# Kernel optimization log

Measured on AMD Instinct MI355X. Metric: run time of the kernel, lower is better.

Reference implementation:

```python
import jax, jax.numpy as jnp
import numpy as np

IN_CH = 64
NODE = 48
K_NEIGS = 10
KERNEL = 5
STRIDE = 2
BN_EPS = 1e-5


def _local_kernel(size, k, s):
    idx = np.arange(size * size).reshape(size, size)
    win = np.lib.stride_tricks.sliding_window_view(idx, (k, k))[::s, ::s]
    patches = win.reshape(-1, k * k)  # [n_edges, k*k] pixel indices
    n_edges = patches.shape[0]
    H = np.zeros((size * size, n_edges), dtype=np.float32)
    H[patches.reshape(-1), np.repeat(np.arange(n_edges), k * k)] = 1.0
    return jnp.asarray(H)


def _pairwise_distance(x):
    # (B,N,C) -> (B,N,N) squared euclidean
    xsq = jnp.sum(x * x, axis=-1, keepdims=True)
    return xsq - 2.0 * jnp.einsum('bnc,bmc->bnm', x, x) + jnp.swapaxes(xsq, 1, 2)


def _batched_knn(x, k):
    d = _pairwise_distance(x)
    avg = d.mean(-1, keepdims=True)
    neg_vals, inds = jax.lax.top_k(-d, k + 1)  # smallest k+1, sorted ascending
    return -neg_vals, inds, d, avg


def _incidence(inds, N):
    # weights_function(prob=False) == ones; scatter ones then transpose
    B, _, K = inds.shape
    b = jnp.arange(B)[:, None, None]
    p = jnp.arange(N)[None, :, None]
    M = jnp.zeros((B, N, N), dtype=jnp.float32).at[b, p, inds].set(1.0)
    return jnp.swapaxes(M, 1, 2)


def _generate_G(H):
    # G = diag(DV^-0.5) @ H @ I @ diag(DE^-1) @ H^T @ diag(DV^-0.5)
    DV = H.sum(axis=2)  # (B,N)
    DE = H.sum(axis=1)  # (B,E)
    dv2 = DV ** -0.5
    Hs = H * (1.0 / DE)[:, None, :]
    M = jnp.einsum('bne,bme->bnm', Hs, H)
    return dv2[:, :, None] * M * dv2[:, None, :]


def _build_G(x, local_H):
    B, N, C = x.shape
    _, topk_inds, _, _ = _batched_knn(x, K_NEIGS)
    H1 = _incidence(topk_inds, N)
    Dv = H1.sum(axis=2, keepdims=True)  # alpha = 1.0
    max_k = int(jnp.max(Dv))  # data-dependent width (eager, matches torch)
    _, ti2, _, _ = _batched_knn(x, max_k - 1)  # (B,N,max_k)
    tk = jnp.arange(max_k)[None, None, :]
    rng = jnp.broadcast_to(jnp.arange(N)[None, :, None], (B, N, max_k))
    new_inds = jnp.where(tk >= Dv, rng, ti2)
    new_H = _incidence(new_inds, N)
    loc = jnp.broadcast_to(local_H[None], (B,) + local_H.shape)
    return _generate_G(jnp.concatenate([new_H, loc], axis=2))


def _hgnn(x, G, W, b, gamma, beta):
    h = jnp.einsum('bnc,oc->bno', x, W) + b  # Linear
    h = jnp.einsum('bnm,bmc->bnc', G, h)
    mean = h.mean(axis=(0, 1))  # BatchNorm1d over (B,N) per channel
    var = h.var(axis=(0, 1))
    h = gamma * (h - mean) / jnp.sqrt(var + BN_EPS) + beta
    return jax.nn.relu(h) + x


def setup_inputs() -> dict:
    key = jax.random.key(0)
    k1, k2, k3 = jax.random.split(key, 3)
    B, N, C = 4, NODE * NODE, IN_CH
    x = jax.random.normal(k1, (B, N, C), dtype=jnp.float32)
    W = jax.random.normal(k2, (C, C), dtype=jnp.float32) / np.sqrt(C)
    b = jax.random.normal(k3, (C,), dtype=jnp.float32) * 0.01
    gamma = jnp.ones((C,), dtype=jnp.float32)
    beta = jnp.zeros((C,), dtype=jnp.float32)
    return {"x": x, "W": W, "b": b, "gamma": gamma, "beta": beta}


def reference(x, W, b, gamma, beta):
    local_H = _local_kernel(NODE, KERNEL, STRIDE)
    G = _build_G(x, local_H)  # graph construction is no_grad in torch
    return _hgnn(x, G, W, b, gamma, beta)
```

## Files before the change

kernel.cpp:

```cpp
#include <hip/hip_runtime.h>


#define HB    4
#define HN    2304
#define HC    64
#define HK    11
#define HL    48
#define HW    22
#define HE2   484
#define HE    (HN + HE2)
#define HRPB  4
#define NSLOT 36
#define NPAIRS (HB * HK * HN)

__global__ void hg14_sentinel(float* out, int n) {
    int i = blockIdx.x * 256 + threadIdx.x;
    if (i < n) out[i] = 12345.0f;
}

__global__ void hg14_init(int* Dv, int* indeg, float* bnsum, float* bnss) {
    int i = blockIdx.x * 256 + threadIdx.x;
    if (i < HB * HN) { Dv[i] = 0; indeg[i] = 0; }
    if (i < HC) { bnsum[i] = 0.f; bnss[i] = 0.f; }
}

__global__ __launch_bounds__(64) void hg14_linear(const float* x, const float* W,
                                                  const float* bias, float* h1,
                                                  float* xsq, float* xT) {
    int row = blockIdx.x;
    int t = threadIdx.x;
    __shared__ float xr[HC];
    float v = x[row * HC + t];
    xr[t] = v;
    __syncthreads();
    float sq = v * v;
    #pragma unroll
    for (int o = 32; o > 0; o >>= 1) sq += __shfl_xor(sq, o);
    if (t == 0) xsq[row] = sq;
    int b = row / HN, n = row % HN;
    xT[(b * HC + t) * HN + n] = v;
    float acc = bias[t];
    #pragma unroll 8
    for (int c = 0; c < HC; c++) acc += xr[c] * W[t * HC + c];
    h1[row * HC + t] = acc;
}

__device__ __forceinline__ unsigned hg14_wave_min_u32(unsigned v) {
    #pragma unroll
    for (int o = 32; o > 0; o >>= 1) {
        unsigned ov = __shfl_xor(v, o);
        v = ov < v ? ov : v;
    }
    return v;
}

#define HG14_INS4(q0, q1, q2, q3, x)                                     \
    {                                                                    \
        unsigned long long x_ = (x), n_;                                 \
        n_ = q0 < x_ ? q0 : x_; x_ = q0 < x_ ? x_ : q0; q0 = n_;         \
        n_ = q1 < x_ ? q1 : x_; x_ = q1 < x_ ? x_ : q1; q1 = n_;         \
        n_ = q2 < x_ ? q2 : x_; x_ = q2 < x_ ? x_ : q2; q2 = n_;         \
        if (x_ < q3) q3 = x_;                                            \
    }

#define HG14_CE(u, v)                                                    \
    { unsigned long long t_ = u < v ? u : v; v = u < v ? v : u; u = t_; }

#define HG14_BUILD()                                                               \
    {                                                                              \
        unsigned long long a0 = CINF, a1 = CINF, a2 = CINF, a3 = CINF;             \
        unsigned long long b0 = CINF, b1 = CINF, b2 = CINF, b3 = CINF;             \
        _Pragma("unroll")                                                          \
        for (int s = 0; s < NSLOT / 2; s++) {                                      \
            unsigned long long pa = ((unsigned long long)key[s] << 12) |           \
                                    (unsigned)((s << 6) | lane);                   \
            unsigned long long pb = ((unsigned long long)key[s + 18] << 12) |      \
                                    (unsigned)(((s + 18) << 6) | lane);            \
            HG14_INS4(a0, a1, a2, a3, pa);                                         \
            HG14_INS4(b0, b1, b2, b3, pb);                                         \
        }                                                                          \
        c0 = a0 < b3 ? a0 : b3; c1 = a1 < b2 ? a1 : b2;                            \
        c2 = a2 < b1 ? a2 : b1; c3 = a3 < b0 ? a3 : b0;                            \
        HG14_CE(c0, c2); HG14_CE(c1, c3); HG14_CE(c0, c1); HG14_CE(c2, c3);        \
    }

#define HG14_EXTRACT(kk, EMIT)                                                     \
    {                                                                              \
        for (int j = 0; j < (kk); j++) {                                           \
            unsigned hk = (unsigned)(c0 >> 12);                                    \
            unsigned mk = hg14_wave_min_u32(hk);                                   \
            unsigned long long bal = __ballot(hk == mk);                           \
            bool iswin;                                                            \
            if (__popcll(bal) == 1) {                                              \
                iswin = (hk == mk);                                                \
            } else {                                                               \
                unsigned mc = (hk == mk) ? (unsigned)(c0 & 0xFFFu) : 0xFFFFFFFFu;  \
                unsigned mm = hg14_wave_min_u32(mc);                               \
                iswin = (mc == mm);                                                \
            }                                                                      \
            if (iswin) {                                                           \
                int bi = (int)(c0 & 0xFFFu);                                       \
                EMIT;                                                              \
                unsigned long long popped = c0;                                    \
                c0 = c1; c1 = c2; c2 = c3; c3 = CINF;                              \
                if (c0 == CINF) {                                                  \
                    _Pragma("unroll")                                              \
                    for (int s = 0; s < NSLOT; s++) {                              \
                        unsigned long long pk =                                    \
                            ((unsigned long long)key[s] << 12) |                   \
                            (unsigned)((s << 6) | lane);                           \
                        if (pk > popped) HG14_INS4(c0, c1, c2, c3, pk);            \
                    }                                                              \
                }                                                                  \
            }                                                                      \
        }                                                                          \
    }

__device__ __forceinline__ void hg14_kth(const unsigned (&key)[NSLOT], int kk,
                                         unsigned& T, int& cntLess, int& take) {
    unsigned andv = 0xFFFFFFFFu, orv = 0u;
    #pragma unroll
    for (int s = 0; s < NSLOT; s++) { andv &= key[s]; orv |= key[s]; }
    #pragma unroll
    for (int o = 32; o > 0; o >>= 1) {
        andv &= (unsigned)__shfl_xor((int)andv, o);
        orv  |= (unsigned)__shfl_xor((int)orv, o);
    }
    unsigned diff = andv ^ orv;
    if (diff == 0u) { T = andv; cntLess = 0; take = kk; return; }
    int tstart = 31 - __builtin_clz(diff);
    unsigned lowmask = (tstart == 31) ? 0xFFFFFFFFu : ((1u << (tstart + 1)) - 1u);
    unsigned pref = andv & ~lowmask;
    int r = kk;
    for (int t = tstart; t >= 0; t--) {
        unsigned pt = pref >> t;
        int c = 0;
        #pragma unroll
        for (int s = 0; s < NSLOT; s++) c += ((key[s] >> t) == pt) ? 1 : 0;
        #pragma unroll
        for (int o = 32; o > 0; o >>= 1) c += __shfl_xor(c, o);
        if (r > c) { r -= c; pref |= (1u << t); }
    }
    T = pref; cntLess = kk - r; take = r;
}

__device__ __forceinline__ void hg14_scan64(int v, int lane, int& excl, int& total) {
    int inc = v;
    #pragma unroll
    for (int o = 1; o < 64; o <<= 1) {
        int u = __shfl_up(inc, o);
        if (lane >= o) inc += u;
    }
    excl = inc - v;
    total = __shfl(inc, 63);
}

__global__ __launch_bounds__(256) void hg14_knn_count(const float* xT, const float* xsq,
                                                      int* Dv, unsigned int* kcache,
                                                      int storekeys) {
    __shared__ float d[HRPB][HN];
    __shared__ __align__(16) float xrt[HC][HRPB];
    const int t = threadIdx.x;
    const int b = blockIdx.x / (HN / HRPB);
    const int n0 = (blockIdx.x % (HN / HRPB)) * HRPB;
    const int r = t >> 6;
    const int lane = t & 63;
    xrt[lane][r] = xT[(b * HC + lane) * HN + n0 + r];
    __syncthreads();
    float xs[HRPB];
    #pragma unroll
    for (int q = 0; q < HRPB; q++) xs[q] = xsq[b * HN + n0 + q];

    #pragma unroll
    for (int i = 0; i < 4; i++) {
        const int m = 512 * i + 2 * t;
        float2 d0 = {0.f, 0.f}, d1 = {0.f, 0.f}, d2 = {0.f, 0.f}, d3 = {0.f, 0.f};
        #pragma unroll 8
        for (int c = 0; c < HC; c++) {
            float4 xq = *reinterpret_cast<const float4*>(&xrt[c][0]);
            float2 xv = *reinterpret_cast<const float2*>(&xT[(b * HC + c) * HN + m]);
            d0.x += xq.x * xv.x; d0.y += xq.x * xv.y;
            d1.x += xq.y * xv.x; d1.y += xq.y * xv.y;
            d2.x += xq.z * xv.x; d2.y += xq.z * xv.y;
            d3.x += xq.w * xv.x; d3.y += xq.w * xv.y;
        }
        float s0 = xsq[b * HN + m], s1 = xsq[b * HN + m + 1];
        *reinterpret_cast<float2*>(&d[0][m]) =
            make_float2(xs[0] + s0 - 2.f * d0.x, xs[0] + s1 - 2.f * d0.y);
        *reinterpret_cast<float2*>(&d[1][m]) =
            make_float2(xs[1] + s0 - 2.f * d1.x, xs[1] + s1 - 2.f * d1.y);
        *reinterpret_cast<float2*>(&d[2][m]) =
            make_float2(xs[2] + s0 - 2.f * d2.x, xs[2] + s1 - 2.f * d2.y);
        *reinterpret_cast<float2*>(&d[3][m]) =
            make_float2(xs[3] + s0 - 2.f * d3.x, xs[3] + s1 - 2.f * d3.y);
    }
    {
        const int m = 2048 + t;
        float d0 = 0.f, d1 = 0.f, d2 = 0.f, d3 = 0.f;
        #pragma unroll 8
        for (int c = 0; c < HC; c++) {
            float4 xq = *reinterpret_cast<const float4*>(&xrt[c][0]);
            float xv = xT[(b * HC + c) * HN + m];
            d0 += xq.x * xv; d1 += xq.y * xv; d2 += xq.z * xv; d3 += xq.w * xv;
        }
        float sm = xsq[b * HN + m];
        d[0][m] = xs[0] + sm - 2.f * d0;
        d[1][m] = xs[1] + sm - 2.f * d1;
        d[2][m] = xs[2] + sm - 2.f * d2;
        d[3][m] = xs[3] + sm - 2.f * d3;
    }
    __syncthreads();

    const int p = n0 + r;
    const unsigned long long CINF = ~0ull;
    unsigned int key[NSLOT];
    unsigned long long c0, c1, c2, c3;
    const int rowbase = (b * HN + p) * NSLOT;
    #pragma unroll
    for (int s = 0; s < NSLOT; s++) {
        float f = d[r][(s << 6) | lane];
        unsigned int ub = __float_as_uint(f);
        unsigned int k = ub ^ (((unsigned int)(((int)ub) >> 31)) | 0x80000000u);
        key[s] = k;
        if (storekeys) kcache[(rowbase + s) * 64 + lane] = k;
    }
    HG14_BUILD();
    HG14_EXTRACT(HK, atomicAdd(&Dv[b * HN + bi], 1));
}

__global__ __launch_bounds__(256) void hg14_scan(const int* Dv, int* offs) {
    __shared__ int part[256];
    int t = threadIdx.x;
    int base = t * 36;
    int s = 0;
    for (int i = 0; i < 36; i++) s += max(Dv[base + i], 1);
    part[t] = s;
    __syncthreads();
    if (t == 0) { int acc = 0; for (int i = 0; i < 256; i++) { int v = part[i]; part[i] = acc; acc += v; } }
    __syncthreads();
    int acc = part[t];
    for (int i = 0; i < 36; i++) { offs[base + i] = acc; acc += max(Dv[base + i], 1); }
}

__device__ __forceinline__ void hg14_select_emit(const unsigned (&key)[NSLOT],
                                                 int b, int p, int lane, int kk, int base,
                                                 int* indeg, unsigned int* pairs) {
    unsigned T; int cntLess, take;
    hg14_kth(key, kk, T, cntLess, take);
    int cl = 0;
    #pragma unroll
    for (int s = 0; s < NSLOT; s++) cl += (key[s] < T) ? 1 : 0;
    int off, tot;
    hg14_scan64(cl, lane, off, tot);
    int w = 0;
    #pragma unroll
    for (int s = 0; s < NSLOT; s++) {
        if (key[s] < T) {
            int m = (s << 6) | lane;
            atomicAdd(&indeg[b * HN + m], 1);
            pairs[base + off + w] =
                ((unsigned)b << 24) | ((unsigned)p << 12) | (unsigned)m;
            w++;
        }
    }
    int lastm = -1;
    for (int t2 = 0; t2 < take; t2++) {
        int mc = 0x7FFFFFFF;
        #pragma unroll
        for (int s = 0; s < NSLOT; s++) {
            int m = (s << 6) | lane;
            if (key[s] == T && m > lastm && m < mc) mc = m;
        }
        int mmin = mc;
        #pragma unroll
        for (int o = 32; o > 0; o >>= 1) {
            int ov = __shfl_xor(mmin, o);
            mmin = ov < mmin ? ov : mmin;
        }
        if (mc == mmin) {
            atomicAdd(&indeg[b * HN + mmin], 1);
            pairs[base + cntLess + t2] =
                ((unsigned)b << 24) | ((unsigned)p << 12) | (unsigned)mmin;
        }
        lastm = mmin;
    }
}

__global__ __launch_bounds__(256) void hg14_knn_sel_cached(const unsigned int* kcache,
                                                           const int* Dv, const int* offs,
                                                           int* indeg, unsigned int* pairs) {
    const int t = threadIdx.x;
    const int lane = t & 63;
    const int gw = blockIdx.x * HRPB + (t >> 6);
    const int b = gw / HN, p = gw % HN;
    unsigned int key[NSLOT];
    const int rowbase = gw * NSLOT;
    #pragma unroll
    for (int s = 0; s < NSLOT; s++) key[s] = kcache[(rowbase + s) * 64 + lane];
    hg14_select_emit(key, b, p, lane, max(Dv[gw], 1), offs[gw], indeg, pairs);
}

__global__ __launch_bounds__(256) void hg14_knn_sel_full(const float* xT, const float* xsq,
                                                         const int* Dv, const int* offs,
                                                         int* indeg, unsigned int* pairs) {
    __shared__ float d[HRPB][HN];
    __shared__ float xr[HRPB][HC];
    const int t = threadIdx.x;
    const int b = blockIdx.x / (HN / HRPB);
    const int n0 = (blockIdx.x % (HN / HRPB)) * HRPB;
    const int r = t >> 6;
    const int lane = t & 63;
    xr[r][lane] = xT[(b * HC + lane) * HN + n0 + r];
    __syncthreads();
    float xs[HRPB];
    #pragma unroll
    for (int q = 0; q < HRPB; q++) xs[q] = xsq[b * HN + n0 + q];
    for (int m = t; m < HN; m += 256) {
        float dot0 = 0.f, dot1 = 0.f, dot2 = 0.f, dot3 = 0.f;
        #pragma unroll 8
        for (int c = 0; c < HC; c++) {
            float xv = xT[(b * HC + c) * HN + m];
            dot0 += xr[0][c] * xv;
            dot1 += xr[1][c] * xv;
            dot2 += xr[2][c] * xv;
            dot3 += xr[3][c] * xv;
        }
        float xsm = xsq[b * HN + m];
        d[0][m] = xs[0] + xsm - 2.f * dot0;
        d[1][m] = xs[1] + xsm - 2.f * dot1;
        d[2][m] = xs[2] + xsm - 2.f * dot2;
        d[3][m] = xs[3] + xsm - 2.f * dot3;
    }
    __syncthreads();
    const int p = n0 + r;
    unsigned int key[NSLOT];
    #pragma unroll
    for (int s = 0; s < NSLOT; s++) {
        float f = d[r][(s << 6) | lane];
        unsigned int ub = __float_as_uint(f);
        key[s] = ub ^ (((unsigned int)(((int)ub) >> 31)) | 0x80000000u);
    }
    const int gw = b * HN + p;
    hg14_select_emit(key, b, p, lane, max(Dv[gw], 1), offs[gw], indeg, pairs);
}

__device__ __forceinline__ int hg14_lo(int rc) { return max(0, (rc - 3) / 2); }
__device__ __forceinline__ int hg14_hi(int rc) { return min(HW - 1, rc / 2); }

__global__ __launch_bounds__(256) void hg14_scale(float* h1, const int* indeg) {
    int i = blockIdx.x * 256 + threadIdx.x;
    int node = i >> 6;
    int n = node % HN;
    int r = n / HL, c = n % HL;
    int cover = max(0, hg14_hi(r) - hg14_lo(r) + 1) * max(0, hg14_hi(c) - hg14_lo(c) + 1);
    int dvn = max(indeg[node] + cover, 1);
    h1[i] *= rsqrtf((float)dvn);
}

__global__ void hg14_zero(float* z, float* h2) {
    int i = blockIdx.x * 256 + threadIdx.x;
    int b = i / (HN * HC), rem = i % (HN * HC);
    z[b * HE * HC + rem] = 0.f;
    h2[i] = 0.f;
}

__global__ __launch_bounds__(256) void hg14_edge(const unsigned int* pairs, const int* Dv,
                                                 const float* y, float* z) {
    int wv = (blockIdx.x * 256 + threadIdx.x) >> 6;
    int lane = threadIdx.x & 63;
    if (wv < NPAIRS) {
        unsigned int pk = pairs[wv];
        int b = pk >> 24;
        if (b >= HB) return;
        int p = (pk >> 12) & 0xFFF, m = pk & 0xFFF;
        float invde = 1.f / (float)max(Dv[b * HN + p], 1);
        atomicAdd(&z[(b * HE + p) * HC + lane], y[(b * HN + m) * HC + lane] * invde);
    } else {
        int w2 = wv - NPAIRS;
        if (w2 >= HB * HE2) return;
        int b = w2 / HE2, w = w2 % HE2;
        int wr = w / HW, wc = w % HW;
        float acc = 0.f;
        #pragma unroll
        for (int i = 0; i < 5; i++)
            #pragma unroll
            for (int j = 0; j < 5; j++)
                acc += y[(b * HN + (wr * 2 + i) * HL + wc * 2 + j) * HC + lane];
        z[(b * HE + HN + w) * HC + lane] = acc * (1.f / 25.f);
    }
}

__global__ __launch_bounds__(256) void hg14_gscatter(const unsigned int* pairs,
                                                     const float* z, float* h2) {
    int idx = (blockIdx.x * 256 + threadIdx.x) >> 6;
    int lane = threadIdx.x & 63;
    if (idx >= NPAIRS) return;
    unsigned int pk = pairs[idx];
    int b = pk >> 24;
    if (b >= HB) return;
    int p = (pk >> 12) & 0xFFF, m = pk & 0xFFF;
    atomicAdd(&h2[(b * HN + m) * HC + lane], z[(b * HE + p) * HC + lane]);
}

__global__ __launch_bounds__(256) void hg14_gfinish(const float* z, const int* indeg, float* h2) {
    int wave = (blockIdx.x * 256 + threadIdx.x) >> 6;
    int lane = threadIdx.x & 63;
    int b = wave / HN, n = wave % HN;
    int g = b * HN + n;
    float acc = h2[g * HC + lane];
    int r = n / HL, c = n % HL;
    int rlo = hg14_lo(r), rhi = hg14_hi(r), clo = hg14_lo(c), chi = hg14_hi(c);
    for (int wr = rlo; wr <= rhi; wr++)
        for (int wc = clo; wc <= chi; wc++)
            acc += z[(b * HE + HN + wr * HW + wc) * HC + lane];
    int dvn = max(indeg[g] + max(0, rhi - rlo + 1) * max(0, chi - clo + 1), 1);
    h2[g * HC + lane] = acc * rsqrtf((float)dvn);
}

__global__ __launch_bounds__(256) void hg14_bnstats(const float* h2, float* bnsum, float* bnss) {
    int t = threadIdx.x;
    int c = t & 63, rg = t >> 6;
    int row0 = blockIdx.x * 36;
    float s = 0.f, ss = 0.f;
    for (int r = rg; r < 36; r += 4) {
        float v = h2[(row0 + r) * HC + c];
        s += v; ss += v * v;
    }
    __shared__ float ls[256], lss[256];
    ls[t] = s; lss[t] = ss;
    __syncthreads();
    if (t < 64) {
        s  = ls[t]  + ls[t + 64]  + ls[t + 128]  + ls[t + 192];
        ss = lss[t] + lss[t + 64] + lss[t + 128] + lss[t + 192];
        atomicAdd(&bnsum[t], s);
        atomicAdd(&bnss[t], ss);
    }
}

__global__ __launch_bounds__(256) void hg14_final(const float* h2, const float* x,
                                                  const float* gamma, const float* beta,
                                                  const float* bnsum, const float* bnss,
                                                  float* out) {
    int i = blockIdx.x * 256 + threadIdx.x;
    int c = i & 63;
    const float M = (float)(HB * HN);
    float mean = bnsum[c] / M;
    float var  = bnss[c] / M - mean * mean;
    float inv  = rsqrtf(var + 1e-5f);
    float h = gamma[c] * (h2[i] - mean) * inv + beta[c];
    out[i] = fmaxf(h, 0.f) + x[i];
}

extern "C" void kernel_launch(void* const* d_in, const int* in_sizes, int n_in,
                              void* d_out, int out_size, void* d_ws, size_t ws_size,
                              hipStream_t stream) {
    const float* x     = (const float*)d_in[0];
    const float* W     = (const float*)d_in[1];
    const float* bias  = (const float*)d_in[2];
    const float* gamma = (const float*)d_in[3];
    const float* beta  = (const float*)d_in[4];
    float* out = (float*)d_out;
    (void)in_sizes; (void)n_in;

    char* ws = (char*)d_ws;
    size_t off = 0;
    float*        xsq     = (float*)(ws + off);        off += (size_t)HB * HN * 4;
    float*        h1      = (float*)(ws + off);        off += (size_t)HB * HN * HC * 4;
    float*        h2      = (float*)(ws + off);        off += (size_t)HB * HN * HC * 4;
    int*          Dv      = (int*)(ws + off);          off += (size_t)HB * HN * 4;
    int*          indeg   = (int*)(ws + off);          off += (size_t)HB * HN * 4;
    int*          offs    = (int*)(ws + off);          off += (size_t)HB * HN * 4;
    unsigned int* pairs   = (unsigned int*)(ws + off); off += (size_t)NPAIRS * 4;
    float*        bnsum   = (float*)(ws + off);        off += 256;
    float*        bnss    = (float*)(ws + off);        off += 256;
    float*        xT      = (float*)(ws + off);
    float*        z       = (float*)(ws + off);
    off += (size_t)HB * HE * HC * 4;
    size_t base_need = off;
    unsigned int* kcache  = (unsigned int*)(ws + off);
    size_t cache_need = off + (size_t)HB * HN * NSLOT * 64 * 4;

    if (ws_size < base_need) {
        hg14_sentinel<<<(out_size + 255) / 256, 256, 0, stream>>>(out, out_size);
        return;
    }
    const int use_cache = (ws_size >= cache_need) ? 1 : 0;

    const int EDGE_WAVES = NPAIRS + HB * HE2;

    hg14_init<<<(HB * HN + 255) / 256, 256, 0, stream>>>(Dv, indeg, bnsum, bnss);
    hg14_linear<<<HB * HN, 64, 0, stream>>>(x, W, bias, h1, xsq, xT);
    hg14_knn_count<<<HB * (HN / HRPB), 256, 0, stream>>>(xT, xsq, Dv, kcache, use_cache);
    hg14_scan<<<1, 256, 0, stream>>>(Dv, offs);
    if (use_cache)
        hg14_knn_sel_cached<<<HB * (HN / HRPB), 256, 0, stream>>>(kcache, Dv, offs, indeg, pairs);
    else
        hg14_knn_sel_full<<<HB * (HN / HRPB), 256, 0, stream>>>(xT, xsq, Dv, offs, indeg, pairs);
    hg14_scale<<<(HB * HN * HC) / 256, 256, 0, stream>>>(h1, indeg);
    hg14_zero<<<(HB * HN * HC) / 256, 256, 0, stream>>>(z, h2);
    hg14_edge<<<EDGE_WAVES / 4, 256, 0, stream>>>(pairs, Dv, h1, z);
    hg14_gscatter<<<(NPAIRS * 64) / 256, 256, 0, stream>>>(pairs, z, h2);
    hg14_gfinish<<<(HB * HN) / 4, 256, 0, stream>>>(z, indeg, h2);
    hg14_bnstats<<<256, 256, 0, stream>>>(h2, bnsum, bnss);
    hg14_final<<<(HB * HN * HC) / 256, 256, 0, stream>>>(h2, x, gamma, beta, bnsum, bnss, out);
}
```

Before: 375.2 us.

## Cache per-row top-192 candidates instead of full distance keys for KNN selection

Instead of writing all 2304 sort keys per row to a global cache and rereading them in the selection pass, the count kernel now picks the 192 smallest keys per row and stores them packed with their column indices. The selection kernel reads only those 192 candidates. Rows whose degree exceeds the cap fall back to a kernel that recomputes the distances. The scale and zero kernels are also merged into one prep kernel. This cuts global traffic in the select pass, at the cost of extra kth-selection work in the count kernel and an extra, mostly idle, fallback launch.

```diff
diff --git a/kernel.cpp b/kernel.cpp
--- a/kernel.cpp
+++ b/kernel.cpp
@@ -11,20 +11,21 @@
 #define HE    (HN + HE2)
 #define HRPB  4
 #define NSLOT 36
+#define HCAP  192
 #define NPAIRS (HB * HK * HN)
 
-__global__ void hg14_sentinel(float* out, int n) {
+__global__ void hg16_sentinel(float* out, int n) {
     int i = blockIdx.x * 256 + threadIdx.x;
     if (i < n) out[i] = 12345.0f;
 }
 
-__global__ void hg14_init(int* Dv, int* indeg, float* bnsum, float* bnss) {
+__global__ void hg16_init(int* Dv, int* indeg, float* bnsum, float* bnss) {
     int i = blockIdx.x * 256 + threadIdx.x;
     if (i < HB * HN) { Dv[i] = 0; indeg[i] = 0; }
     if (i < HC) { bnsum[i] = 0.f; bnss[i] = 0.f; }
 }
 
-__global__ __launch_bounds__(64) void hg14_linear(const float* x, const float* W,
+__global__ __launch_bounds__(64) void hg16_linear(const float* x, const float* W,
                                                   const float* bias, float* h1,
                                                   float* xsq, float* xT) {
     int row = blockIdx.x;
@@ -45,7 +46,7 @@
     h1[row * HC + t] = acc;
 }
 
-__device__ __forceinline__ unsigned hg14_wave_min_u32(unsigned v) {
+__device__ __forceinline__ unsigned hg16_wave_min_u32(unsigned v) {
     #pragma unroll
     for (int o = 32; o > 0; o >>= 1) {
         unsigned ov = __shfl_xor(v, o);
@@ -54,7 +55,7 @@
     return v;
 }
 
-#define HG14_INS4(q0, q1, q2, q3, x)                                     \
+#define HG16_INS4(q0, q1, q2, q3, x)                                     \
     {                                                                    \
         unsigned long long x_ = (x), n_;                                 \
         n_ = q0 < x_ ? q0 : x_; x_ = q0 < x_ ? x_ : q0; q0 = n_;         \
@@ -63,10 +64,10 @@
         if (x_ < q3) q3 = x_;                                            \
     }
 
-#define HG14_CE(u, v)                                                    \
+#define HG16_CE(u, v)                                                    \
     { unsigned long long t_ = u < v ? u : v; v = u < v ? v : u; u = t_; }
 
-#define HG14_BUILD()                                                               \
+#define HG16_BUILD()                                                               \
     {                                                                              \
         unsigned long long a0 = CINF, a1 = CINF, a2 = CINF, a3 = CINF;             \
         unsigned long long b0 = CINF, b1 = CINF, b2 = CINF, b3 = CINF;             \
@@ -76,26 +77,26 @@
                                     (unsigned)((s << 6) | lane);                   \
             unsigned long long pb = ((unsigned long long)key[s + 18] << 12) |      \
                                     (unsigned)(((s + 18) << 6) | lane);            \
-            HG14_INS4(a0, a1, a2, a3, pa);                                         \
-            HG14_INS4(b0, b1, b2, b3, pb);                                         \
+            HG16_INS4(a0, a1, a2, a3, pa);                                         \
+            HG16_INS4(b0, b1, b2, b3, pb);                                         \
         }                                                                          \
         c0 = a0 < b3 ? a0 : b3; c1 = a1 < b2 ? a1 : b2;                            \
         c2 = a2 < b1 ? a2 : b1; c3 = a3 < b0 ? a3 : b0;                            \
-        HG14_CE(c0, c2); HG14_CE(c1, c3); HG14_CE(c0, c1); HG14_CE(c2, c3);        \
-    }
-
-#define HG14_EXTRACT(kk, EMIT)                                                     \
+        HG16_CE(c0, c2); HG16_CE(c1, c3); HG16_CE(c0, c1); HG16_CE(c2, c3);        \
+    }
+
+#define HG16_EXTRACT(kk, EMIT)                                                     \
     {                                                                              \
         for (int j = 0; j < (kk); j++) {                                           \
             unsigned hk = (unsigned)(c0 >> 12);                                    \
-            unsigned mk = hg14_wave_min_u32(hk);                                   \
+            unsigned mk = hg16_wave_min_u32(hk);                                   \
             unsigned long long bal = __ballot(hk == mk);                           \
             bool iswin;                                                            \
             if (__popcll(bal) == 1) {                                              \
                 iswin = (hk == mk);                                                \
             } else {                                                               \
                 unsigned mc = (hk == mk) ? (unsigned)(c0 & 0xFFFu) : 0xFFFFFFFFu;  \
-                unsigned mm = hg14_wave_min_u32(mc);                               \
+                unsigned mm = hg16_wave_min_u32(mc);                               \
                 iswin = (mc == mm);                                                \
             }                                                                      \
             if (iswin) {                                                           \
@@ -109,18 +110,19 @@
                         unsigned long long pk =                                    \
                             ((unsigned long long)key[s] << 12) |                   \
                             (unsigned)((s << 6) | lane);                           \
-                        if (pk > popped) HG14_INS4(c0, c1, c2, c3, pk);            \
+                        if (pk > popped) HG16_INS4(c0, c1, c2, c3, pk);            \
                     }                                                              \
                 }                                                                  \
             }                                                                      \
         }                                                                          \
     }
 
-__device__ __forceinline__ void hg14_kth(const unsigned (&key)[NSLOT], int kk,
+template <int NS>
+__device__ __forceinline__ void hg16_kth(const unsigned (&key)[NS], int kk,
                                          unsigned& T, int& cntLess, int& take) {
     unsigned andv = 0xFFFFFFFFu, orv = 0u;
     #pragma unroll
-    for (int s = 0; s < NSLOT; s++) { andv &= key[s]; orv |= key[s]; }
+    for (int s = 0; s < NS; s++) { andv &= key[s]; orv |= key[s]; }
     #pragma unroll
     for (int o = 32; o > 0; o >>= 1) {
         andv &= (unsigned)__shfl_xor((int)andv, o);
@@ -136,7 +138,7 @@
         unsigned pt = pref >> t;
         int c = 0;
         #pragma unroll
-        for (int s = 0; s < NSLOT; s++) c += ((key[s] >> t) == pt) ? 1 : 0;
+        for (int s = 0; s < NS; s++) c += ((key[s] >> t) == pt) ? 1 : 0;
         #pragma unroll
         for (int o = 32; o > 0; o >>= 1) c += __shfl_xor(c, o);
         if (r > c) { r -= c; pref |= (1u << t); }
@@ -144,7 +146,7 @@
     T = pref; cntLess = kk - r; take = r;
 }
 
-__device__ __forceinline__ void hg14_scan64(int v, int lane, int& excl, int& total) {
+__device__ __forceinline__ void hg16_scan64(int v, int lane, int& excl, int& total) {
     int inc = v;
     #pragma unroll
     for (int o = 1; o < 64; o <<= 1) {
@@ -155,9 +157,8 @@
     total = __shfl(inc, 63);
 }
 
-__global__ __launch_bounds__(256) void hg14_knn_count(const float* xT, const float* xsq,
-                                                      int* Dv, unsigned int* kcache,
-                                                      int storekeys) {
+__global__ __launch_bounds__(256) void hg16_knn_count(const float* xT, const float* xsq,
+                                                      int* Dv, unsigned long long* topc) {
     __shared__ float d[HRPB][HN];
     __shared__ __align__(16) float xrt[HC][HRPB];
     const int t = threadIdx.x;
@@ -212,23 +213,56 @@
     __syncthreads();
 
     const int p = n0 + r;
+    const int gw = b * HN + p;
     const unsigned long long CINF = ~0ull;
     unsigned int key[NSLOT];
     unsigned long long c0, c1, c2, c3;
-    const int rowbase = (b * HN + p) * NSLOT;
     #pragma unroll
     for (int s = 0; s < NSLOT; s++) {
         float f = d[r][(s << 6) | lane];
         unsigned int ub = __float_as_uint(f);
-        unsigned int k = ub ^ (((unsigned int)(((int)ub) >> 31)) | 0x80000000u);
-        key[s] = k;
-        if (storekeys) kcache[(rowbase + s) * 64 + lane] = k;
-    }
-    HG14_BUILD();
-    HG14_EXTRACT(HK, atomicAdd(&Dv[b * HN + bi], 1));
-}
-
-__global__ __launch_bounds__(256) void hg14_scan(const int* Dv, int* offs) {
+        key[s] = ub ^ (((unsigned int)(((int)ub) >> 31)) | 0x80000000u);
+    }
+    HG16_BUILD();
+    HG16_EXTRACT(HK, atomicAdd(&Dv[b * HN + bi], 1));
+    unsigned T; int cntLess, take;
+    hg16_kth<NSLOT>(key, HCAP, T, cntLess, take);
+    int cl = 0;
+    #pragma unroll
+    for (int s = 0; s < NSLOT; s++) cl += (key[s] < T) ? 1 : 0;
+    int off, tot;
+    hg16_scan64(cl, lane, off, tot);
+    unsigned long long* tb = topc + (size_t)gw * HCAP;
+    int w = 0;
+    #pragma unroll
+    for (int s = 0; s < NSLOT; s++) {
+        if (key[s] < T) {
+            tb[off + w] = ((unsigned long long)key[s] << 12)
+                        | (unsigned)((s << 6) | lane);
+            w++;
+        }
+    }
+    int lastm = -1;
+    for (int t2 = 0; t2 < take; t2++) {
+        int mc = 0x7FFFFFFF;
+        #pragma unroll
+        for (int s = 0; s < NSLOT; s++) {
+            int m = (s << 6) | lane;
+            if (key[s] == T && m > lastm && m < mc) mc = m;
+        }
+        int mmin = mc;
+        #pragma unroll
+        for (int o = 32; o > 0; o >>= 1) {
+            int ov = __shfl_xor(mmin, o);
+            mmin = ov < mmin ? ov : mmin;
+        }
+        if (mc == mmin)
+            tb[cntLess + t2] = ((unsigned long long)T << 12) | (unsigned)mmin;
+        lastm = mmin;
+    }
+}
+
+__global__ __launch_bounds__(256) void hg16_scan(const int* Dv, int* offs) {
     __shared__ int part[256];
     int t = threadIdx.x;
     int base = t * 36;
@@ -242,21 +276,35 @@
     for (int i = 0; i < 36; i++) { offs[base + i] = acc; acc += max(Dv[base + i], 1); }
 }
 
-__device__ __forceinline__ void hg14_select_emit(const unsigned (&key)[NSLOT],
-                                                 int b, int p, int lane, int kk, int base,
-                                                 int* indeg, unsigned int* pairs) {
+__global__ __launch_bounds__(256) void hg16_sel_top(const unsigned long long* topc,
+                                                    const int* Dv, const int* offs,
+                                                    int* indeg, unsigned int* pairs) {
+    const int t = threadIdx.x;
+    const int lane = t & 63;
+    const int gw = blockIdx.x * HRPB + (t >> 6);
+    const int b = gw / HN, p = gw % HN;
+    const int kk = max(Dv[gw], 1);
+    if (kk > HCAP) return;
+    unsigned long long pk[3];
+    unsigned key[3];
+    #pragma unroll
+    for (int s = 0; s < 3; s++) {
+        pk[s] = topc[(size_t)gw * HCAP + (s << 6) + lane];
+        key[s] = (unsigned)(pk[s] >> 12);
+    }
     unsigned T; int cntLess, take;
-    hg14_kth(key, kk, T, cntLess, take);
+    hg16_kth<3>(key, kk, T, cntLess, take);
+    const int base = offs[gw];
     int cl = 0;
     #pragma unroll
-    for (int s = 0; s < NSLOT; s++) cl += (key[s] < T) ? 1 : 0;
+    for (int s = 0; s < 3; s++) cl += (key[s] < T) ? 1 : 0;
     int off, tot;
-    hg14_scan64(cl, lane, off, tot);
+    hg16_scan64(cl, lane, off, tot);
     int w = 0;
     #pragma unroll
-    for (int s = 0; s < NSLOT; s++) {
+    for (int s = 0; s < 3; s++) {
         if (key[s] < T) {
-            int m = (s << 6) | lane;
+            int m = (int)(pk[s] & 0xFFFu);
             atomicAdd(&indeg[b * HN + m], 1);
             pairs[base + off + w] =
                 ((unsigned)b << 24) | ((unsigned)p << 12) | (unsigned)m;
@@ -267,8 +315,8 @@
     for (int t2 = 0; t2 < take; t2++) {
         int mc = 0x7FFFFFFF;
         #pragma unroll
-        for (int s = 0; s < NSLOT; s++) {
-            int m = (s << 6) | lane;
+        for (int s = 0; s < 3; s++) {
+            int m = (int)(pk[s] & 0xFFFu);
             if (key[s] == T && m > lastm && m < mc) mc = m;
         }
         int mmin = mc;
@@ -286,28 +334,19 @@
     }
 }
 
-__global__ __launch_bounds__(256) void hg14_knn_sel_cached(const unsigned int* kcache,
-                                                           const int* Dv, const int* offs,
-                                                           int* indeg, unsigned int* pairs) {
-    const int t = threadIdx.x;
-    const int lane = t & 63;
-    const int gw = blockIdx.x * HRPB + (t >> 6);
-    const int b = gw / HN, p = gw % HN;
-    unsigned int key[NSLOT];
-    const int rowbase = gw * NSLOT;
-    #pragma unroll
-    for (int s = 0; s < NSLOT; s++) key[s] = kcache[(rowbase + s) * 64 + lane];
-    hg14_select_emit(key, b, p, lane, max(Dv[gw], 1), offs[gw], indeg, pairs);
-}
-
-__global__ __launch_bounds__(256) void hg14_knn_sel_full(const float* xT, const float* xsq,
-                                                         const int* Dv, const int* offs,
-                                                         int* indeg, unsigned int* pairs) {
-    __shared__ float d[HRPB][HN];
-    __shared__ float xr[HRPB][HC];
+__global__ __launch_bounds__(256) void hg16_sel_fullfb(const float* xT, const float* xsq,
+                                                       const int* Dv, const int* offs,
+                                                       int* indeg, unsigned int* pairs) {
     const int t = threadIdx.x;
     const int b = blockIdx.x / (HN / HRPB);
     const int n0 = (blockIdx.x % (HN / HRPB)) * HRPB;
+    bool need = false;
+    #pragma unroll
+    for (int q = 0; q < HRPB; q++) need |= (Dv[b * HN + n0 + q] > HCAP);
+    if (!need) return;
+
+    __shared__ float d[HRPB][HN];
+    __shared__ float xr[HRPB][HC];
     const int r = t >> 6;
     const int lane = t & 63;
     xr[r][lane] = xT[(b * HC + lane) * HN + n0 + r];
@@ -333,6 +372,9 @@
     }
     __syncthreads();
     const int p = n0 + r;
+    const int gw = b * HN + p;
+    const int kk = max(Dv[gw], 1);
+    if (kk <= HCAP) return;
     unsigned int key[NSLOT];
     #pragma unroll
     for (int s = 0; s < NSLOT; s++) {
@@ -340,31 +382,66 @@
         unsigned int ub = __float_as_uint(f);
         key[s] = ub ^ (((unsigned int)(((int)ub) >> 31)) | 0x80000000u);
     }
-    const int gw = b * HN + p;
-    hg14_select_emit(key, b, p, lane, max(Dv[gw], 1), offs[gw], indeg, pairs);
-}
-
-__device__ __forceinline__ int hg14_lo(int rc) { return max(0, (rc - 3) / 2); }
-__device__ __forceinline__ int hg14_hi(int rc) { return min(HW - 1, rc / 2); }
-
-__global__ __launch_bounds__(256) void hg14_scale(float* h1, const int* indeg) {
+    unsigned T; int cntLess, take;
+    hg16_kth<NSLOT>(key, kk, T, cntLess, take);
+    const int base = offs[gw];
+    int cl = 0;
+    #pragma unroll
+    for (int s = 0; s < NSLOT; s++) cl += (key[s] < T) ? 1 : 0;
+    int off, tot;
+    hg16_scan64(cl, lane, off, tot);
+    int w = 0;
+    #pragma unroll
+    for (int s = 0; s < NSLOT; s++) {
+        if (key[s] < T) {
+            int m = (s << 6) | lane;
+            atomicAdd(&indeg[b * HN + m], 1);
+            pairs[base + off + w] =
+                ((unsigned)b << 24) | ((unsigned)p << 12) | (unsigned)m;
+            w++;
+        }
+    }
+    int lastm = -1;
+    for (int t2 = 0; t2 < take; t2++) {
+        int mc = 0x7FFFFFFF;
+        #pragma unroll
+        for (int s = 0; s < NSLOT; s++) {
+            int m = (s << 6) | lane;
+            if (key[s] == T && m > lastm && m < mc) mc = m;
+        }
+        int mmin = mc;
+        #pragma unroll
+        for (int o = 32; o > 0; o >>= 1) {
+            int ov = __shfl_xor(mmin, o);
+            mmin = ov < mmin ? ov : mmin;
+        }
+        if (mc == mmin) {
+            atomicAdd(&indeg[b * HN + mmin], 1);
+            pairs[base + cntLess + t2] =
+                ((unsigned)b << 24) | ((unsigned)p << 12) | (unsigned)mmin;
+        }
+        lastm = mmin;
+    }
+}
+
+__device__ __forceinline__ int hg16_lo(int rc) { return max(0, (rc - 3) / 2); }
+__device__ __forceinline__ int hg16_hi(int rc) { return min(HW - 1, rc / 2); }
+
+__global__ __launch_bounds__(256) void hg16_prep(float* h1, const int* indeg,
+                                                 float* z, float* h2) {
     int i = blockIdx.x * 256 + threadIdx.x;
     int node = i >> 6;
     int n = node % HN;
     int r = n / HL, c = n % HL;
-    int cover = max(0, hg14_hi(r) - hg14_lo(r) + 1) * max(0, hg14_hi(c) - hg14_lo(c) + 1);
+    int cover = max(0, hg16_hi(r) - hg16_lo(r) + 1) * max(0, hg16_hi(c) - hg16_lo(c) + 1);
     int dvn = max(indeg[node] + cover, 1);
     h1[i] *= rsqrtf((float)dvn);
-}
-
-__global__ void hg14_zero(float* z, float* h2) {
-    int i = blockIdx.x * 256 + threadIdx.x;
     int b = i / (HN * HC), rem = i % (HN * HC);
     z[b * HE * HC + rem] = 0.f;
     h2[i] = 0.f;
 }
 
-__global__ __launch_bounds__(256) void hg14_edge(const unsigned int* pairs, const int* Dv,
+__global__ __launch_bounds__(256) void hg16_edge(const unsigned int* pairs, const int* Dv,
                                                  const float* y, float* z) {
     int wv = (blockIdx.x * 256 + threadIdx.x) >> 6;
     int lane = threadIdx.x & 63;
@@ -390,7 +467,7 @@
     }
 }
 
-__global__ __launch_bounds__(256) void hg14_gscatter(const unsigned int* pairs,
+__global__ __launch_bounds__(256) void hg16_gscatter(const unsigned int* pairs,
                                                      const float* z, float* h2) {
     int idx = (blockIdx.x * 256 + threadIdx.x) >> 6;
     int lane = threadIdx.x & 63;
@@ -402,14 +479,14 @@
     atomicAdd(&h2[(b * HN + m) * HC + lane], z[(b * HE + p) * HC + lane]);
 }
 
-__global__ __launch_bounds__(256) void hg14_gfinish(const float* z, const int* indeg, float* h2) {
+__global__ __launch_bounds__(256) void hg16_gfinish(const float* z, const int* indeg, float* h2) {
     int wave = (blockIdx.x * 256 + threadIdx.x) >> 6;
     int lane = threadIdx.x & 63;
     int b = wave / HN, n = wave % HN;
     int g = b * HN + n;
     float acc = h2[g * HC + lane];
     int r = n / HL, c = n % HL;
-    int rlo = hg14_lo(r), rhi = hg14_hi(r), clo = hg14_lo(c), chi = hg14_hi(c);
+    int rlo = hg16_lo(r), rhi = hg16_hi(r), clo = hg16_lo(c), chi = hg16_hi(c);
     for (int wr = rlo; wr <= rhi; wr++)
         for (int wc = clo; wc <= chi; wc++)
             acc += z[(b * HE + HN + wr * HW + wc) * HC + lane];
@@ -417,7 +494,7 @@
     h2[g * HC + lane] = acc * rsqrtf((float)dvn);
 }
 
-__global__ __launch_bounds__(256) void hg14_bnstats(const float* h2, float* bnsum, float* bnss) {
+__global__ __launch_bounds__(256) void hg16_bnstats(const float* h2, float* bnsum, float* bnss) {
     int t = threadIdx.x;
     int c = t & 63, rg = t >> 6;
     int row0 = blockIdx.x * 36;
@@ -437,7 +514,7 @@
     }
 }
 
-__global__ __launch_bounds__(256) void hg14_final(const float* h2, const float* x,
+__global__ __launch_bounds__(256) void hg16_final(const float* h2, const float* x,
                                                   const float* gamma, const float* beta,
                                                   const float* bnsum, const float* bnss,
                                                   float* out) {
@@ -464,43 +541,37 @@
 
     char* ws = (char*)d_ws;
     size_t off = 0;
-    float*        xsq     = (float*)(ws + off);        off += (size_t)HB * HN * 4;
-    float*        h1      = (float*)(ws + off);        off += (size_t)HB * HN * HC * 4;
-    float*        h2      = (float*)(ws + off);        off += (size_t)HB * HN * HC * 4;
-    int*          Dv      = (int*)(ws + off);          off += (size_t)HB * HN * 4;
-    int*          indeg   = (int*)(ws + off);          off += (size_t)HB * HN * 4;
-    int*          offs    = (int*)(ws + off);          off += (size_t)HB * HN * 4;
-    unsigned int* pairs   = (unsigned int*)(ws + off); off += (size_t)NPAIRS * 4;
-    float*        bnsum   = (float*)(ws + off);        off += 256;
-    float*        bnss    = (float*)(ws + off);        off += 256;
-    float*        xT      = (float*)(ws + off);
-    float*        z       = (float*)(ws + off);
+    float*              xsq   = (float*)(ws + off);              off += (size_t)HB * HN * 4;
+    float*              h1    = (float*)(ws + off);              off += (size_t)HB * HN * HC * 4;
+    float*              h2    = (float*)(ws + off);              off += (size_t)HB * HN * HC * 4;
+    int*                Dv    = (int*)(ws + off);                off += (size_t)HB * HN * 4;
+    int*                indeg = (int*)(ws + off);                off += (size_t)HB * HN * 4;
+    int*                offs  = (int*)(ws + off);                off += (size_t)HB * HN * 4;
+    unsigned int*       pairs = (unsigned int*)(ws + off);       off += (size_t)NPAIRS * 4;
+    float*              bnsum = (float*)(ws + off);              off += 256;
+    float*              bnss  = (float*)(ws + off);              off += 256;
+    unsigned long long* topc  = (unsigned long long*)(ws + off); off += (size_t)HB * HN * HCAP * 8;
+    float*              xT    = (float*)(ws + off);
+    float*              z     = (float*)(ws + off);
     off += (size_t)HB * HE * HC * 4;
-    size_t base_need = off;
-    unsigned int* kcache  = (unsigned int*)(ws + off);
-    size_t cache_need = off + (size_t)HB * HN * NSLOT * 64 * 4;
-
-    if (ws_size < base_need) {
-        hg14_sentinel<<<(out_size + 255) / 256, 256, 0, stream>>>(out, out_size);
+
+    if (ws_size < off) {
+        hg16_sentinel<<<(out_size + 255) / 256, 256, 0, stream>>>(out, out_size);
         return;
     }
-    const int use_cache = (ws_size >= cache_need) ? 1 : 0;
 
     const int EDGE_WAVES = NPAIRS + HB * HE2;
 
-    hg14_init<<<(HB * HN + 255) / 256, 256, 0, stream>>>(Dv, indeg, bnsum, bnss);
-    hg14_linear<<<HB * HN, 64, 0, stream>>>(x, W, bias, h1, xsq, xT);
-    hg14_knn_count<<<HB * (HN / HRPB), 256, 0, stream>>>(xT, xsq, Dv, kcache, use_cache);
-    hg14_scan<<<1, 256, 0, stream>>>(Dv, offs);
-    if (use_cache)
-        hg14_knn_sel_cached<<<HB * (HN / HRPB), 256, 0, stream>>>(kcache, Dv, offs, indeg, pairs);
-    else
-        hg14_knn_sel_full<<<HB * (HN / HRPB), 256, 0, stream>>>(xT, xsq, Dv, offs, indeg, pairs);
-    hg14_scale<<<(HB * HN * HC) / 256, 256, 0, stream>>>(h1, indeg);
-    hg14_zero<<<(HB * HN * HC) / 256, 256, 0, stream>>>(z, h2);
-    hg14_edge<<<EDGE_WAVES / 4, 256, 0, stream>>>(pairs, Dv, h1, z);
-    hg14_gscatter<<<(NPAIRS * 64) / 256, 256, 0, stream>>>(pairs, z, h2);
-    hg14_gfinish<<<(HB * HN) / 4, 256, 0, stream>>>(z, indeg, h2);
-    hg14_bnstats<<<256, 256, 0, stream>>>(h2, bnsum, bnss);
-    hg14_final<<<(HB * HN * HC) / 256, 256, 0, stream>>>(h2, x, gamma, beta, bnsum, bnss, out);
-}
+    hg16_init<<<(HB * HN + 255) / 256, 256, 0, stream>>>(Dv, indeg, bnsum, bnss);
+    hg16_linear<<<HB * HN, 64, 0, stream>>>(x, W, bias, h1, xsq, xT);
+    hg16_knn_count<<<HB * (HN / HRPB), 256, 0, stream>>>(xT, xsq, Dv, topc);
+    hg16_scan<<<1, 256, 0, stream>>>(Dv, offs);
+    hg16_sel_top<<<HB * (HN / HRPB), 256, 0, stream>>>(topc, Dv, offs, indeg, pairs);
+    hg16_sel_fullfb<<<HB * (HN / HRPB), 256, 0, stream>>>(xT, xsq, Dv, offs, indeg, pairs);
+    hg16_prep<<<(HB * HN * HC) / 256, 256, 0, stream>>>(h1, indeg, z, h2);
+    hg16_edge<<<EDGE_WAVES / 4, 256, 0, stream>>>(pairs, Dv, h1, z);
+    hg16_gscatter<<<(NPAIRS * 64) / 256, 256, 0, stream>>>(pairs, z, h2);
+    hg16_gfinish<<<(HB * HN) / 4, 256, 0, stream>>>(z, indeg, h2);
+    hg16_bnstats<<<256, 256, 0, stream>>>(h2, bnsum, bnss);
+    hg16_final<<<(HB * HN * HC) / 256, 256, 0, stream>>>(h2, x, gamma, beta, bnsum, bnss, out);
+}
```

New measurement: 483.7 us. 1.29x slower.
